# Optimization experiments

Measured on AMD Instinct MI355X. Metric: run time of the kernel, lower is better.

## Reference

```python
import jax, jax.numpy as jnp
import numpy as np

B, T, NM = 128, 2048, 8  # batch, nSteps, nMaxwell


def setup_inputs() -> dict:
    key = jax.random.key(0)
    k1, k2, k3 = jax.random.split(key, 3)
    S_e = jax.random.normal(k1, (B, T, 3, 3), dtype=jnp.float32)
    # strictly increasing times per batch element
    dt = jax.random.uniform(k2, (B, T), minval=0.01, maxval=0.1, dtype=jnp.float32)
    t = jnp.cumsum(dt, axis=1)
    # [tau_1..tau_nM, g_infy, g_1..g_nM] -> last dim 2*NM + 1
    PronyParams = jax.random.uniform(k3, (B, T, 2 * NM + 1), minval=0.1, maxval=1.0, dtype=jnp.float32)
    return {"S_e": S_e, "t": t, "PronyParams": PronyParams}


def reference(S_e, t, PronyParams):
    """Viscoelastic 2nd Piola-Kirchhoff stress via recursive Prony update.

    S_e:         [B, T, 3, 3] instantaneous elastic stress
    t:           [B, T] time
    PronyParams: [B, T, 2*nM+1] (relaxation times tau then coefficients g)
    Returns (S, S_infy, Q_sum), each [B, T, 3, 3].
    """
    nM = PronyParams.shape[-1] // 2
    tau = PronyParams[..., :nM]                      # [B,T,nM]
    g = PronyParams[..., nM:]                        # [B,T,nM+1]
    g = g / jnp.sum(g, axis=-1, keepdims=True)
    g_infy = g[..., 0:1]                             # [B,T,1]
    g_i = g[..., 1:]                                 # [B,T,nM]

    Bsz = S_e.shape[0]
    # time-major scan inputs
    xs = (
        jnp.swapaxes(t, 0, 1),      # [T,B]
        jnp.swapaxes(S_e, 0, 1),    # [T,B,3,3]
        jnp.swapaxes(tau, 0, 1),    # [T,B,nM]
        jnp.swapaxes(g_i, 0, 1),    # [T,B,nM]
    )
    init = (
        jnp.zeros((Bsz, nM, 3, 3), S_e.dtype),  # Q_0
        -t[:, 1],                                # t_prev (as in original initializer)
        jnp.zeros((Bsz, 3, 3), S_e.dtype),       # S_prev
        tau[:, 0],
        g_i[:, 0],
    )

    def step(carry, x):
        Q_p, t_p, S_p, tau_p, g_p = carry
        t_c, S_c, tau_c, g_c = x
        g_bar = 0.5 * (g_c + g_p)                 # [B,nM]
        tau_bar = 0.5 * (tau_c + tau_p)           # [B,nM]
        dt = (t_c - t_p)[:, None]                 # [B,1]
        e = jnp.exp(-0.5 * dt / tau_bar)          # exp(-dt/(2 tau_bar))
        term1 = (e * e)[..., None, None]          # exp(-dt/tau_bar), [B,nM,1,1]
        term2 = (e * g_bar)[..., None, None]      # [B,nM,1,1]
        dS = (S_c - S_p)[:, None]                 # [B,1,3,3]
        Q = term1 * Q_p + term2 * dS              # [B,nM,3,3]
        return (Q, t_c, S_c, tau_c, g_c), Q

    _, Qs = jax.lax.scan(step, init, xs)          # [T,B,nM,3,3]
    Q_sum = jnp.swapaxes(jnp.sum(Qs, axis=2), 0, 1)  # [B,T,3,3]
    S_infy = g_infy[..., None] * S_e              # [B,T,1,1] * [B,T,3,3]
    S = S_infy + Q_sum
    return (S, S_infy, Q_sum)
```

## Files before the change

### kernel.cpp

```cpp
#include <hip/hip_runtime.h>

#define T_LEN 2048
#define NMODE 8
#define NPP   17

template <int L, int G>
__global__ __launch_bounds__(256)
void phaseA(const float* __restrict__ Se,
            const float* __restrict__ tt,
            const float* __restrict__ pp,
            float* __restrict__ out,
            float* __restrict__ partR,
            float* __restrict__ partP,
            float* __restrict__ caA,
            int B) {
    constexpr int NC    = T_LEN / L;
    constexpr int NSTEP = G * L;
    constexpr int RW    = NSTEP + 1;
    constexpr int NT    = 256;
    constexpr int RAW_SZ = RW * NPP;
    constexpr int QT_SZ  = 9 * (NSTEP + 4);
    constexpr int CA_K   = L * 8 + 4;
    constexpr int UNION_SZ = (RAW_SZ > QT_SZ + 8 * CA_K) ? RAW_SZ
                                                         : (QT_SZ + 8 * CA_K);
    constexpr int AC_K  = L * 16 + 4;
    constexpr int O_AC  = UNION_SZ;
    constexpr int O_ST  = O_AC + G * AC_K;
    constexpr int SROW  = NSTEP + 4;
    constexpr int O_T   = O_ST + 9 * SROW;
    constexpr int O_INV = O_T + RW;
    constexpr int O_GI  = O_INV + RW;
    constexpr int TOTAL = O_GI + RW;

    __shared__ __align__(16) float sm[TOTAL];
    float* s_raw = sm;
    float* s_qT  = sm;
    float* s_ca  = sm + QT_SZ;
    float* s_AC  = sm + O_AC;
    float* s_ST  = sm + O_ST;
    float* s_t   = sm + O_T;
    float* s_inv = sm + O_INV;
    float* s_gi  = sm + O_GI;

    const int tid  = threadIdx.x;
    const int ngrp = NC / G;
    const int b    = blockIdx.x / ngrp;
    const int grp  = blockIdx.x % ngrp;
    const int c0   = grp * G;
    const int base = c0 * L;
    const int off  = (base == 0) ? 0 : 1;
    const int r0   = (base == 0) ? 0 : base - 1;

    {
        const float* pr = pp + ((size_t)b * T_LEN + r0) * NPP;
        for (int i = tid; i < RW * NPP; i += NT) s_raw[i] = pr[i];
        const float* sr = Se + ((size_t)b * T_LEN + r0) * 9;
        for (int i = tid; i < RW * 9; i += NT) {
            int r = i / 9, e = i - r * 9;
            s_ST[e * SROW + r] = sr[i];
        }
        const float* tr = tt + (size_t)b * T_LEN + r0;
        for (int i = tid; i < RW; i += NT) s_t[i] = tr[i];
    }
    __syncthreads();

    for (int i = tid; i < RW; i += NT) {
        float gs = 0.f;
        #pragma unroll
        for (int k = 8; k < NPP; ++k) gs += s_raw[i * NPP + k];
        float iv = __builtin_amdgcn_rcpf(gs);
        s_inv[i] = iv;
        s_gi[i]  = s_raw[i * NPP + 8] * iv;
    }
    __syncthreads();

    for (int i = tid; i < NSTEP * 8; i += NT) {
        int m  = i & 7;
        int ts = i >> 3;
        int rc = ts + off;
        bool first = (base == 0) && (ts == 0);
        int rp = first ? rc : rc - 1;
        float tau_c = s_raw[rc * NPP + m];
        float tau_p = s_raw[rp * NPP + m];
        float gqh_c = 0.5f * s_raw[rc * NPP + 9 + m] * s_inv[rc];
        float gqh_p = 0.5f * s_raw[rp * NPP + 9 + m] * s_inv[rp];
        float t_c = s_t[rc];
        float t_p = first ? -s_t[1] : s_t[rp];
        float ee  = __expf((t_p - t_c) * __builtin_amdgcn_rcpf(tau_c + tau_p));
        int kk = ts / L, sl = ts % L;
        s_AC[kk * AC_K + sl * 16 + m]     = ee * ee;
        s_AC[kk * AC_K + sl * 16 + 8 + m] = ee * (gqh_c + gqh_p);
    }
    __syncthreads();

    const size_t nOut = (size_t)B * T_LEN * 9;

    if (tid < 72) {
        const int k  = tid / 9;
        const int e  = tid - k * 9;
        const int cg = c0 + k;
        float S_p = (cg == 0) ? 0.f : s_ST[e * SROW + (k * L + off - 1)];

        float Q[8] = {0,0,0,0,0,0,0,0};
        float cA[8] = {1,1,1,1,1,1,1,1};
        const float4* acp = (const float4*)(s_AC + k * AC_K);

        float4 a0 = acp[0], a1 = acp[1], c0v = acp[2], c1v = acp[3];
        #pragma unroll
        for (int s = 0; s < L; ++s) {
            float4 na0, na1, nc0, nc1;
            if (s < L - 1) {
                na0 = acp[4*s+4]; na1 = acp[4*s+5];
                nc0 = acp[4*s+6]; nc1 = acp[4*s+7];
            }
            float S_c = s_ST[e * SROW + (k * L + s + off)];
            float dS  = S_c - S_p;
            S_p = S_c;
            Q[0] = a0.x*Q[0] + c0v.x*dS;  Q[1] = a0.y*Q[1] + c0v.y*dS;
            Q[2] = a0.z*Q[2] + c0v.z*dS;  Q[3] = a0.w*Q[3] + c0v.w*dS;
            Q[4] = a1.x*Q[4] + c1v.x*dS;  Q[5] = a1.y*Q[5] + c1v.y*dS;
            Q[6] = a1.z*Q[6] + c1v.z*dS;  Q[7] = a1.w*Q[7] + c1v.w*dS;
            cA[0]*=a0.x; cA[1]*=a0.y; cA[2]*=a0.z; cA[3]*=a0.w;
            cA[4]*=a1.x; cA[5]*=a1.y; cA[6]*=a1.z; cA[7]*=a1.w;
            float qs = ((Q[0]+Q[1])+(Q[2]+Q[3])) + ((Q[4]+Q[5])+(Q[6]+Q[7]));
            s_qT[e * SROW + (k * L + s)] = qs;
            if (e == 0) {
                float4* cw = (float4*)(s_ca + k * CA_K + s * 8);
                cw[0] = make_float4(cA[0], cA[1], cA[2], cA[3]);
                cw[1] = make_float4(cA[4], cA[5], cA[6], cA[7]);
            }
            a0 = na0; a1 = na1; c0v = nc0; c1v = nc1;
        }

        float4* pr4 = (float4*)(partR + ((size_t)(b * 9 + e) * NC + cg) * 8);
        pr4[0] = make_float4(Q[0], Q[1], Q[2], Q[3]);
        pr4[1] = make_float4(Q[4], Q[5], Q[6], Q[7]);
        if (e == 0) {
            float4* pp4 = (float4*)(partP + ((size_t)b * NC + cg) * 8);
            pp4[0] = make_float4(cA[0], cA[1], cA[2], cA[3]);
            pp4[1] = make_float4(cA[4], cA[5], cA[6], cA[7]);
        }
    } else {
        float* o1 = out + nOut + ((size_t)b * T_LEN + base) * 9;
        for (int i = tid - 72; i < NSTEP * 9; i += 184) {
            int t = i / 9, e = i - t * 9;
            int rc = t + off;
            o1[i] = s_gi[rc] * s_ST[e * SROW + rc];
        }
    }
    __syncthreads();

    float* o2 = out + 2 * nOut + ((size_t)b * T_LEN + base) * 9;
    for (int i = tid; i < NSTEP * 9; i += NT) {
        int t = i / 9, e = i - t * 9;
        o2[i] = s_qT[e * SROW + t];
    }
    float* ca = caA + ((size_t)b * NC + c0) * (L * 8);
    for (int i = tid; i < NSTEP * 8; i += NT) {
        int t = i >> 3, m = i & 7;
        int kk = t / L, sl = t % L;
        ca[i] = s_ca[kk * CA_K + sl * 8 + m];
    }
}

template <int K>
__global__ __launch_bounds__(256)
void chunk_scan_wave(float* __restrict__ R, const float* __restrict__ P,
                     int B) {
    constexpr int NC = K * 64;
    int gtid = blockIdx.x * blockDim.x + threadIdx.x;
    int wid  = gtid >> 6;
    int lane = gtid & 63;
    if (wid >= B * 9) return;
    int e = wid % 9;
    int b = wid / 9;

    float* rp       = R + ((size_t)(b * 9 + e) * NC) * NMODE;
    const float* pq = P + ((size_t)b * NC) * NMODE;

    float pk[K][NMODE], rk[K][NMODE];
    float pa[NMODE], ra[NMODE];
    #pragma unroll
    for (int m = 0; m < NMODE; ++m) { pa[m] = 1.f; ra[m] = 0.f; }

    #pragma unroll
    for (int k = 0; k < K; ++k) {
        int c = lane * K + k;
        const float4* rv = (const float4*)(rp + (size_t)c * NMODE);
        const float4* pv = (const float4*)(pq + (size_t)c * NMODE);
        float4 r0 = rv[0], r1 = rv[1], p0 = pv[0], p1 = pv[1];
        rk[k][0]=r0.x; rk[k][1]=r0.y; rk[k][2]=r0.z; rk[k][3]=r0.w;
        rk[k][4]=r1.x; rk[k][5]=r1.y; rk[k][6]=r1.z; rk[k][7]=r1.w;
        pk[k][0]=p0.x; pk[k][1]=p0.y; pk[k][2]=p0.z; pk[k][3]=p0.w;
        pk[k][4]=p1.x; pk[k][5]=p1.y; pk[k][6]=p1.z; pk[k][7]=p1.w;
        #pragma unroll
        for (int m = 0; m < NMODE; ++m) {
            ra[m] = pk[k][m] * ra[m] + rk[k][m];
            pa[m] = pk[k][m] * pa[m];
        }
    }

    #pragma unroll
    for (int d = 1; d < 64; d <<= 1) {
        #pragma unroll
        for (int m = 0; m < NMODE; ++m) {
            float plo = __shfl_up(pa[m], d);
            float rlo = __shfl_up(ra[m], d);
            if (lane >= d) {
                ra[m] = pa[m] * rlo + ra[m];
                pa[m] = pa[m] * plo;
            }
        }
    }

    float z[NMODE];
    #pragma unroll
    for (int m = 0; m < NMODE; ++m) {
        float zz = __shfl_up(ra[m], 1);
        z[m] = (lane == 0) ? 0.f : zz;
    }

    #pragma unroll
    for (int k = 0; k < K; ++k) {
        int c = lane * K + k;
        float4* rv = (float4*)(rp + (size_t)c * NMODE);
        rv[0] = make_float4(z[0], z[1], z[2], z[3]);
        rv[1] = make_float4(z[4], z[5], z[6], z[7]);
        #pragma unroll
        for (int m = 0; m < NMODE; ++m)
            z[m] = pk[k][m] * z[m] + rk[k][m];
    }
}

template <int L, int GC>
__global__ __launch_bounds__(256)
void phaseC(float* __restrict__ out,
            const float* __restrict__ partR,
            const float* __restrict__ caA,
            int B) {
    constexpr int NC = T_LEN / L;
    const int tid  = threadIdx.x;
    const int ngrp = NC / GC;
    const int b  = blockIdx.x / ngrp;
    const int g  = blockIdx.x % ngrp;
    const int c0 = g * GC;

    __shared__ float s_Z[GC * 72];
    __shared__ float s_ca[GC * L * 8];

    for (int i = tid; i < GC * 72; i += 256) {
        int cl = i / 72, u = i % 72, e = u >> 3, m = u & 7;
        s_Z[i] = partR[((size_t)(b * 9 + e) * NC + c0 + cl) * 8 + m];
    }
    const float* ca = caA + ((size_t)b * NC + c0) * (L * 8);
    for (int i = tid; i < GC * L * 8; i += 256) s_ca[i] = ca[i];
    __syncthreads();

    const size_t nOut = (size_t)B * T_LEN * 9;
    float* o = out + ((size_t)b * T_LEN + (size_t)c0 * L) * 9;
    for (int i = tid; i < GC * L * 9; i += 256) {
        int t = i / 9, e = i - t * 9;
        int cl = t / L;
        const float* caT = &s_ca[t * 8];
        const float* zE  = &s_Z[cl * 72 + e * 8];
        float corr = 0.f;
        #pragma unroll
        for (int m = 0; m < NMODE; ++m) corr += caT[m] * zE[m];
        float qs = o[2 * nOut + i] + corr;
        o[i]            = o[nOut + i] + qs;
        o[2 * nOut + i] = qs;
    }
}

extern "C" void kernel_launch(void* const* d_in, const int* in_sizes, int n_in,
                              void* d_out, int out_size, void* d_ws, size_t ws_size,
                              hipStream_t stream) {
    const float* Se = (const float*)d_in[0];
    const float* tt = (const float*)d_in[1];
    const float* pp = (const float*)d_in[2];
    float* out = (float*)d_out;

    int B = in_sizes[1] / T_LEN;

    constexpr int L  = 16;
    constexpr int NC = T_LEN / L;
    constexpr int K  = NC / 64;
    constexpr int G  = 8;
    constexpr int GC = 4;

    float* partR = (float*)d_ws;
    float* partP = partR + (size_t)B * 9 * NC * 8;
    float* caA   = partP + (size_t)B * NC * 8;

    int gridA = B * (NC / G);
    int gridB = (B * 9 * 64 + 255) / 256;
    int gridC = B * (NC / GC);

    phaseA<L, G><<<gridA, dim3(256), 0, stream>>>(
        Se, tt, pp, out, partR, partP, caA, B);
    chunk_scan_wave<K><<<gridB, dim3(256), 0, stream>>>(partR, partP, B);
    phaseC<L, GC><<<gridC, dim3(256), 0, stream>>>(out, partR, caA, B);
}
```

Baseline: 112.5 us.

## Split cumulative-decay product to dedicated threads and vectorize global stores

Phase A precomputes the per-step stress differences into registers, removes the cumulative decay product from the 72 recurrence threads, and gives it to 64 otherwise idle threads that compute it per mode from shared memory. Output stores of Q_sum and the decay table move to float4 writes. Phase C now loads and stores with float4 and doubles the chunks per block. The aim is a shorter serial recurrence and fewer global memory transactions, at the cost of fewer threads writing S_infy and more register use.

Result: faster. 108.4 us (-3.6%).

```diff
diff --git a/kernel.cpp b/kernel.cpp
--- a/kernel.cpp
+++ b/kernel.cpp
@@ -21,12 +21,12 @@
     constexpr int RAW_SZ = RW * NPP;
     constexpr int QT_SZ  = 9 * (NSTEP + 4);
     constexpr int CA_K   = L * 8 + 4;
-    constexpr int UNION_SZ = (RAW_SZ > QT_SZ + 8 * CA_K) ? RAW_SZ
-                                                         : (QT_SZ + 8 * CA_K);
+    constexpr int UNION_SZ = (RAW_SZ > QT_SZ + G * CA_K) ? RAW_SZ
+                                                         : (QT_SZ + G * CA_K);
     constexpr int AC_K  = L * 16 + 4;
     constexpr int O_AC  = UNION_SZ;
+    constexpr int SROW  = NSTEP + 4;
     constexpr int O_ST  = O_AC + G * AC_K;
-    constexpr int SROW  = NSTEP + 4;
     constexpr int O_T   = O_ST + 9 * SROW;
     constexpr int O_INV = O_T + RW;
     constexpr int O_GI  = O_INV + RW;
@@ -99,10 +99,19 @@
         const int k  = tid / 9;
         const int e  = tid - k * 9;
         const int cg = c0 + k;
-        float S_p = (cg == 0) ? 0.f : s_ST[e * SROW + (k * L + off - 1)];
+
+        float dS[L];
+        {
+            float Sv[L + 1];
+            Sv[0] = (cg == 0) ? 0.f : s_ST[e * SROW + (k * L + off - 1)];
+            #pragma unroll
+            for (int s = 0; s < L; ++s)
+                Sv[s + 1] = s_ST[e * SROW + (k * L + s + off)];
+            #pragma unroll
+            for (int s = 0; s < L; ++s) dS[s] = Sv[s + 1] - Sv[s];
+        }
 
         float Q[8] = {0,0,0,0,0,0,0,0};
-        float cA[8] = {1,1,1,1,1,1,1,1};
         const float4* acp = (const float4*)(s_AC + k * AC_K);
 
         float4 a0 = acp[0], a1 = acp[1], c0v = acp[2], c1v = acp[3];
@@ -113,53 +122,61 @@
                 na0 = acp[4*s+4]; na1 = acp[4*s+5];
                 nc0 = acp[4*s+6]; nc1 = acp[4*s+7];
             }
-            float S_c = s_ST[e * SROW + (k * L + s + off)];
-            float dS  = S_c - S_p;
-            S_p = S_c;
-            Q[0] = a0.x*Q[0] + c0v.x*dS;  Q[1] = a0.y*Q[1] + c0v.y*dS;
-            Q[2] = a0.z*Q[2] + c0v.z*dS;  Q[3] = a0.w*Q[3] + c0v.w*dS;
-            Q[4] = a1.x*Q[4] + c1v.x*dS;  Q[5] = a1.y*Q[5] + c1v.y*dS;
-            Q[6] = a1.z*Q[6] + c1v.z*dS;  Q[7] = a1.w*Q[7] + c1v.w*dS;
-            cA[0]*=a0.x; cA[1]*=a0.y; cA[2]*=a0.z; cA[3]*=a0.w;
-            cA[4]*=a1.x; cA[5]*=a1.y; cA[6]*=a1.z; cA[7]*=a1.w;
+            float d = dS[s];
+            Q[0] = a0.x*Q[0] + c0v.x*d;  Q[1] = a0.y*Q[1] + c0v.y*d;
+            Q[2] = a0.z*Q[2] + c0v.z*d;  Q[3] = a0.w*Q[3] + c0v.w*d;
+            Q[4] = a1.x*Q[4] + c1v.x*d;  Q[5] = a1.y*Q[5] + c1v.y*d;
+            Q[6] = a1.z*Q[6] + c1v.z*d;  Q[7] = a1.w*Q[7] + c1v.w*d;
             float qs = ((Q[0]+Q[1])+(Q[2]+Q[3])) + ((Q[4]+Q[5])+(Q[6]+Q[7]));
             s_qT[e * SROW + (k * L + s)] = qs;
-            if (e == 0) {
-                float4* cw = (float4*)(s_ca + k * CA_K + s * 8);
-                cw[0] = make_float4(cA[0], cA[1], cA[2], cA[3]);
-                cw[1] = make_float4(cA[4], cA[5], cA[6], cA[7]);
-            }
             a0 = na0; a1 = na1; c0v = nc0; c1v = nc1;
         }
 
         float4* pr4 = (float4*)(partR + ((size_t)(b * 9 + e) * NC + cg) * 8);
         pr4[0] = make_float4(Q[0], Q[1], Q[2], Q[3]);
         pr4[1] = make_float4(Q[4], Q[5], Q[6], Q[7]);
-        if (e == 0) {
-            float4* pp4 = (float4*)(partP + ((size_t)b * NC + cg) * 8);
-            pp4[0] = make_float4(cA[0], cA[1], cA[2], cA[3]);
-            pp4[1] = make_float4(cA[4], cA[5], cA[6], cA[7]);
-        }
-    } else {
+    } else if (tid < 192) {
         float* o1 = out + nOut + ((size_t)b * T_LEN + base) * 9;
-        for (int i = tid - 72; i < NSTEP * 9; i += 184) {
+        for (int i = tid - 72; i < NSTEP * 9; i += 120) {
             int t = i / 9, e = i - t * 9;
             int rc = t + off;
             o1[i] = s_gi[rc] * s_ST[e * SROW + rc];
         }
+    } else {
+        const int u = tid - 192;
+        const int k = u >> 3;
+        const int m = u & 7;
+        float c = 1.f;
+        #pragma unroll
+        for (int s = 0; s < L; ++s) {
+            c *= s_AC[k * AC_K + s * 16 + m];
+            s_ca[k * CA_K + s * 8 + m] = c;
+        }
+        partP[((size_t)b * NC + (c0 + k)) * 8 + m] = c;
     }
     __syncthreads();
 
     float* o2 = out + 2 * nOut + ((size_t)b * T_LEN + base) * 9;
-    for (int i = tid; i < NSTEP * 9; i += NT) {
-        int t = i / 9, e = i - t * 9;
-        o2[i] = s_qT[e * SROW + t];
+    for (int i4 = tid; i4 < NSTEP * 9 / 4; i4 += NT) {
+        int i = i4 * 4;
+        float4 v;
+        {
+            int t0i = i / 9,     e0i = i - t0i * 9;
+            int t1i = (i+1) / 9, e1i = (i+1) - t1i * 9;
+            int t2i = (i+2) / 9, e2i = (i+2) - t2i * 9;
+            int t3i = (i+3) / 9, e3i = (i+3) - t3i * 9;
+            v.x = s_qT[e0i * SROW + t0i];
+            v.y = s_qT[e1i * SROW + t1i];
+            v.z = s_qT[e2i * SROW + t2i];
+            v.w = s_qT[e3i * SROW + t3i];
+        }
+        ((float4*)o2)[i4] = v;
     }
     float* ca = caA + ((size_t)b * NC + c0) * (L * 8);
-    for (int i = tid; i < NSTEP * 8; i += NT) {
-        int t = i >> 3, m = i & 7;
-        int kk = t / L, sl = t % L;
-        ca[i] = s_ca[kk * CA_K + sl * 8 + m];
+    {
+        int k = tid >> 5, j = tid & 31;
+        const float4* src = (const float4*)(s_ca + k * CA_K);
+        ((float4*)(ca + k * L * 8))[j] = src[j];
     }
 }
 
@@ -239,6 +256,7 @@
             const float* __restrict__ caA,
             int B) {
     constexpr int NC = T_LEN / L;
+    constexpr int NE = GC * L * 9;
     const int tid  = threadIdx.x;
     const int ngrp = NC / GC;
     const int b  = blockIdx.x / ngrp;
@@ -246,29 +264,46 @@
     const int c0 = g * GC;
 
     __shared__ float s_Z[GC * 72];
-    __shared__ float s_ca[GC * L * 8];
+    __shared__ __align__(16) float s_ca[GC * L * 8];
 
     for (int i = tid; i < GC * 72; i += 256) {
         int cl = i / 72, u = i % 72, e = u >> 3, m = u & 7;
         s_Z[i] = partR[((size_t)(b * 9 + e) * NC + c0 + cl) * 8 + m];
     }
-    const float* ca = caA + ((size_t)b * NC + c0) * (L * 8);
-    for (int i = tid; i < GC * L * 8; i += 256) s_ca[i] = ca[i];
+    {
+        const float4* ca4 = (const float4*)(caA + ((size_t)b * NC + c0) * (L * 8));
+        for (int i = tid; i < GC * L * 2; i += 256)
+            ((float4*)s_ca)[i] = ca4[i];
+    }
     __syncthreads();
 
     const size_t nOut = (size_t)B * T_LEN * 9;
     float* o = out + ((size_t)b * T_LEN + (size_t)c0 * L) * 9;
-    for (int i = tid; i < GC * L * 9; i += 256) {
-        int t = i / 9, e = i - t * 9;
-        int cl = t / L;
-        const float* caT = &s_ca[t * 8];
-        const float* zE  = &s_Z[cl * 72 + e * 8];
-        float corr = 0.f;
-        #pragma unroll
-        for (int m = 0; m < NMODE; ++m) corr += caT[m] * zE[m];
-        float qs = o[2 * nOut + i] + corr;
-        o[i]            = o[nOut + i] + qs;
-        o[2 * nOut + i] = qs;
+    const float4* sf4 = (const float4*)(o + nOut);
+    float4* s4 = (float4*)o;
+    float4* q4 = (float4*)(o + 2 * nOut);
+
+    for (int i4 = tid; i4 < NE / 4; i4 += 256) {
+        int i = i4 * 4;
+        float4 qv = q4[i4];
+        float4 fv = sf4[i4];
+        float corr[4];
+        #pragma unroll
+        for (int j = 0; j < 4; ++j) {
+            int t = (i + j) / 9, e = (i + j) - t * 9;
+            int cl = t / L;
+            const float* caT = &s_ca[t * 8];
+            const float* zE  = &s_Z[cl * 72 + e * 8];
+            float cr = 0.f;
+            #pragma unroll
+            for (int m = 0; m < NMODE; ++m) cr += caT[m] * zE[m];
+            corr[j] = cr;
+        }
+        float4 qn = make_float4(qv.x + corr[0], qv.y + corr[1],
+                                qv.z + corr[2], qv.w + corr[3]);
+        q4[i4] = qn;
+        s4[i4] = make_float4(fv.x + qn.x, fv.y + qn.y,
+                             fv.z + qn.z, fv.w + qn.w);
     }
 }
 
@@ -286,7 +321,7 @@
     constexpr int NC = T_LEN / L;
     constexpr int K  = NC / 64;
     constexpr int G  = 8;
-    constexpr int GC = 4;
+    constexpr int GC = 8;
 
     float* partR = (float*)d_ws;
     float* partP = partR + (size_t)B * 9 * NC * 8;
```
